# Kernel tuning notes

Hardware: AMD Instinct MI355X
Metric: run time of the kernel (lower is better)

The kernel has to match this reference:

```python
import jax, jax.numpy as jnp
import numpy as np

B, H, D, K, V, M = 64, 32, 4096, 128, 128, 4095

def setup_inputs() -> dict:
    key = jax.random.key(0)
    ks = jax.random.split(key, 7)
    return {
        "x": jax.random.normal(ks[0], (B, D), dtype=jnp.float32),
        "prev_K": jax.random.normal(ks[1], (B, M, K), dtype=jnp.float32),
        "prev_V": jax.random.normal(ks[2], (B, M, V), dtype=jnp.float32),
        "Wq": jax.random.normal(ks[3], (H, D, K), dtype=jnp.float32),
        "Wk": jax.random.normal(ks[4], (D, K), dtype=jnp.float32),
        "Wv": jax.random.normal(ks[5], (D, V), dtype=jnp.float32),
        "Wo": jax.random.normal(ks[6], (H, V, D), dtype=jnp.float32),
    }

def reference(x, prev_K, prev_V, Wq, Wk, Wv, Wo):
    # Projections
    q = jnp.einsum('bd,hdk->bhk', x, Wq)            # [b,h,k]
    k_new = jnp.einsum('bd,dk->bk', x, Wk)          # [b,k]
    v_new = jnp.einsum('bd,dv->bv', x, Wv)          # [b,v]
    Kc = jnp.concatenate([prev_K, k_new[:, None, :]], axis=1)  # [b,m+1,k]
    Vc = jnp.concatenate([prev_V, v_new[:, None, :]], axis=1)  # [b,m+1,v]
    # Shared-KV attention (MQA)
    logits = jnp.einsum('bhk,bmk->bhm', q, Kc)
    weights = jax.nn.softmax(logits, axis=-1)
    o = jnp.einsum('bhm,bmv->bhv', weights, Vc)
    y = jnp.einsum('bhv,hvd->bd', o, Wo)
    return (y, Kc, Vc)
```

## Files before the change

kernel.cpp:

```cpp
#include <hip/hip_runtime.h>
#include <stdint.h>

#define B_  64
#define H_  32
#define D_  4096
#define KD  128
#define VD  128
#define M_  4095
#define M1_ 4096
#define NCHUNK 32
#define LOG2E 1.44269504088896f

#define WS_P      0ull
#define WS_Q      4456448ull
#define WS_STATS  4718592ull
#define WS_O      4849664ull
#define WS_OPART  5111808ull

#define WAITVL(n) asm volatile("s_waitcnt vmcnt(" #n ") lgkmcnt(0)" ::: "memory")
#define WAITL()  asm volatile("s_waitcnt lgkmcnt(0)" ::: "memory")
#define BAR()    __builtin_amdgcn_s_barrier()

typedef __attribute__((address_space(3))) char lds_char;
typedef const __attribute__((address_space(1))) char glb_char;

__global__ __launch_bounds__(256) void k_proj_partial(
    const float* __restrict__ x, const float* __restrict__ Wq,
    const float* __restrict__ Wk, const float* __restrict__ Wv,
    float* __restrict__ P) {
  __shared__ float xs[64][260];
  const int dc = blockIdx.x;
  const int hx = blockIdx.y;
  const int t  = threadIdx.x;
  const float* xsrc = x + dc * 256;
  #pragma unroll
  for (int j = 0; j < 16; ++j) {
    int f = t + 256 * j;
    int row = f >> 6, c4 = f & 63;
    *(float4*)&xs[row][c4 * 4] =
        *(const float4*)(xsrc + (size_t)row * D_ + c4 * 4);
  }
  __syncthreads();
  const int bq = t >> 4;
  const int kg = t & 15;
  const int b0 = bq * 4;
  const float* W = (hx < H_) ? (Wq + (size_t)hx * D_ * KD)
                             : ((hx == H_) ? Wk : Wv);
  const float* wp = W + (size_t)(dc * 256) * KD + kg * 8;
  float acc[4][8];
  #pragma unroll
  for (int i = 0; i < 4; ++i)
    #pragma unroll
    for (int j = 0; j < 8; ++j) acc[i][j] = 0.f;
  #pragma unroll 8
  for (int d = 0; d < 256; ++d) {
    float4 w0 = *(const float4*)(wp + (size_t)d * KD);
    float4 w1 = *(const float4*)(wp + (size_t)d * KD + 4);
    float xv[4];
    #pragma unroll
    for (int i = 0; i < 4; ++i) xv[i] = xs[b0 + i][d];
    #pragma unroll
    for (int i = 0; i < 4; ++i) {
      acc[i][0] += xv[i] * w0.x; acc[i][1] += xv[i] * w0.y;
      acc[i][2] += xv[i] * w0.z; acc[i][3] += xv[i] * w0.w;
      acc[i][4] += xv[i] * w1.x; acc[i][5] += xv[i] * w1.y;
      acc[i][6] += xv[i] * w1.z; acc[i][7] += xv[i] * w1.w;
    }
  }
  #pragma unroll
  for (int i = 0; i < 4; ++i) {
    size_t base = ((size_t)(dc * 64 + b0 + i) * 34 + hx) * KD + kg * 8;
    *(float4*)&P[base]     = make_float4(acc[i][0], acc[i][1], acc[i][2], acc[i][3]);
    *(float4*)&P[base + 4] = make_float4(acc[i][4], acc[i][5], acc[i][6], acc[i][7]);
  }
}

__global__ __launch_bounds__(256) void k_proj_reduce(
    const float* __restrict__ P, float* __restrict__ q,
    float* __restrict__ Kc, float* __restrict__ Vc) {
  int i = blockIdx.x * 256 + threadIdx.x;
  int k = i & 127;
  int hx = (i >> 7) % 34;
  int b = i / (128 * 34);
  float s = 0.f;
  #pragma unroll
  for (int dc = 0; dc < 16; ++dc)
    s += P[(size_t)dc * (64 * 34 * 128) + (size_t)(b * 34 + hx) * 128 + k];
  if (hx < H_)       q[((size_t)b * H_ + hx) * KD + k] = s;
  else if (hx == H_) Kc[((size_t)b * M1_ + M_) * KD + k] = s;
  else               Vc[((size_t)b * M1_ + M_) * VD + k] = s;
}

__device__ __forceinline__ void stage_issue(
    const float* src, const float* app_row, float* lbuf, int m_lo, int t) {
  const int wb = t & ~63;
  #pragma unroll
  for (int j = 0; j < 4; ++j) {
    int f = j * 256 + t;
    int r = f >> 5, p = f & 31;
    int m = m_lo + r;
    int g4 = p ^ (r & 7);
    const float* gp = (m < M_) ? (src + (size_t)m * 128 + g4 * 4)
                               : (app_row + g4 * 4);
    __builtin_amdgcn_global_load_lds(
        (glb_char*)gp, (lds_char*)(lbuf + (size_t)(j * 256 + wb) * 4),
        16, 0, 0);
  }
}

__device__ __forceinline__ void copy_out(
    const float* lbuf, float* dst, int m_lo, int t) {
  #pragma unroll
  for (int jj = 0; jj < 4; ++jj) {
    int f = jj * 256 + t;
    int r = f >> 5, p = f & 31;
    int g4 = p ^ (r & 7);
    float4 v = *(const float4*)&lbuf[(size_t)f * 4];
    *(float4*)(dst + (size_t)(m_lo + r) * 128 + g4 * 4) = v;
  }
}

__global__ __launch_bounds__(256, 3) void k_flash(
    const float* __restrict__ prevK, const float* __restrict__ prevV,
    const float* __restrict__ q, float* __restrict__ Kc, float* __restrict__ Vc,
    float* __restrict__ o_part, float* __restrict__ stats) {
  __shared__ float buf[2][32 * 128];
  __shared__ float upool[4608];
  const int chunk = blockIdx.x;
  const int b = blockIdx.y;
  const int t = threadIdx.x;
  const int m0 = chunk * 128;

  const float* kbase = prevK + (size_t)b * M_ * KD;
  const float* vbase = prevV + (size_t)b * M_ * VD;
  const float* kapp  = Kc + ((size_t)b * M1_ + M_) * KD;
  const float* vapp  = Vc + ((size_t)b * M1_ + M_) * VD;
  float* kc = Kc + (size_t)b * M1_ * KD;
  float* vc = Vc + (size_t)b * M1_ * VD;

  const float* qsrc = q + (size_t)b * H_ * KD;
  float4 qv4[4];
  #pragma unroll
  for (int j = 0; j < 4; ++j) {
    int f = j * 256 + t;
    qv4[j] = *(const float4*)(qsrc + (size_t)(f >> 5) * KD + (f & 31) * 4);
  }
  stage_issue(kbase, kapp, buf[0], m0, t);
  #pragma unroll
  for (int j = 0; j < 4; ++j) {
    int f = j * 256 + t;
    *(float4*)&upool[(f >> 5) * 132 + (f & 31) * 4] = qv4[j];
  }

  const int mg = t & 15, hg = t >> 4, h0 = hg * 2;
  const int v4 = t & 31, hoct = t >> 5, h0v = hoct * 4;

  float accL0[8], accL1[8];

#define LOGITS_TILE(S, BUFI)                                                  \
  {                                                                           \
    const float* lb = buf[BUFI];                                              \
    float c00 = 0.f, c01 = 0.f, c10 = 0.f, c11 = 0.f;                         \
    const int sw = (mg & 7);                                                  \
    _Pragma("unroll 4")                                                       \
    for (int k4 = 0; k4 < 32; ++k4) {                                         \
      int p = (k4 ^ sw) * 4;                                                  \
      float4 qa = *(const float4*)&upool[h0 * 132 + k4 * 4];                  \
      float4 qb = *(const float4*)&upool[(h0 + 1) * 132 + k4 * 4];            \
      float4 k0v = *(const float4*)&lb[mg * 128 + p];                         \
      float4 k1v = *(const float4*)&lb[(mg + 16) * 128 + p];                  \
      c00 += qa.x*k0v.x + qa.y*k0v.y + qa.z*k0v.z + qa.w*k0v.w;               \
      c01 += qa.x*k1v.x + qa.y*k1v.y + qa.z*k1v.z + qa.w*k1v.w;               \
      c10 += qb.x*k0v.x + qb.y*k0v.y + qb.z*k0v.z + qb.w*k0v.w;               \
      c11 += qb.x*k1v.x + qb.y*k1v.y + qb.z*k1v.z + qb.w*k1v.w;               \
    }                                                                         \
    accL0[(S) * 2]     = c00;                                                 \
    accL0[(S) * 2 + 1] = c01;                                                 \
    accL1[(S) * 2]     = c10;                                                 \
    accL1[(S) * 2 + 1] = c11;                                                 \
  }

#define PV_TILE(S, BUFI)                                                      \
  {                                                                           \
    const float* lb = buf[BUFI];                                              \
    _Pragma("unroll 4")                                                       \
    for (int mm = 0; mm < 32; ++mm) {                                         \
      int p = (v4 ^ (mm & 7)) * 4;                                            \
      float4 gv = *(const float4*)&lb[mm * 128 + p];                          \
      float4 w4 = *(const float4*)&upool[((S) * 32 + mm) * 36 + h0v];         \
      a0.x += w4.x*gv.x; a0.y += w4.x*gv.y; a0.z += w4.x*gv.z; a0.w += w4.x*gv.w; \
      a1.x += w4.y*gv.x; a1.y += w4.y*gv.y; a1.z += w4.y*gv.z; a1.w += w4.y*gv.w; \
      a2.x += w4.z*gv.x; a2.y += w4.z*gv.y; a2.z += w4.z*gv.z; a2.w += w4.z*gv.w; \
      a3.x += w4.w*gv.x; a3.y += w4.w*gv.y; a3.z += w4.w*gv.z; a3.w += w4.w*gv.w; \
    }                                                                         \
  }

  stage_issue(kbase, kapp, buf[1], m0 + 32, t);
  WAITVL(4); BAR();
  LOGITS_TILE(0, 0);
  copy_out(buf[0], kc, m0, t);
  WAITL(); BAR();

  stage_issue(kbase, kapp, buf[0], m0 + 64, t);
  WAITVL(8); BAR();
  LOGITS_TILE(1, 1);
  copy_out(buf[1], kc, m0 + 32, t);
  WAITL(); BAR();

  stage_issue(kbase, kapp, buf[1], m0 + 96, t);
  WAITVL(8); BAR();
  LOGITS_TILE(2, 0);
  copy_out(buf[0], kc, m0 + 64, t);
  WAITL(); BAR();

  stage_issue(vbase, vapp, buf[0], m0, t);
  WAITVL(8); BAR();
  LOGITS_TILE(3, 1);
  copy_out(buf[1], kc, m0 + 96, t);
  WAITL(); BAR();

  {
    float mx0 = -3.402823466e38f, mx1 = -3.402823466e38f;
    #pragma unroll
    for (int j = 0; j < 8; ++j) {
      mx0 = fmaxf(mx0, accL0[j]);
      mx1 = fmaxf(mx1, accL1[j]);
    }
    #pragma unroll
    for (int off = 1; off <= 8; off <<= 1) {
      mx0 = fmaxf(mx0, __shfl_xor(mx0, off));
      mx1 = fmaxf(mx1, __shfl_xor(mx1, off));
    }
    float s0 = 0.f, s1 = 0.f;
    #pragma unroll
    for (int j = 0; j < 8; ++j) {
      float e0 = exp2f((accL0[j] - mx0) * LOG2E); accL0[j] = e0; s0 += e0;
      float e1 = exp2f((accL1[j] - mx1) * LOG2E); accL1[j] = e1; s1 += e1;
    }
    #pragma unroll
    for (int off = 1; off <= 8; off <<= 1) {
      s0 += __shfl_xor(s0, off);
      s1 += __shfl_xor(s1, off);
    }
    #pragma unroll
    for (int s = 0; s < 4; ++s)
      #pragma unroll
      for (int i = 0; i < 2; ++i) {
        int m = s * 32 + mg + 16 * i;
        upool[m * 36 + h0]     = accL0[s * 2 + i];
        upool[m * 36 + h0 + 1] = accL1[s * 2 + i];
      }
    if (mg == 0) {
      size_t sb0 = (((size_t)b * H_ + h0) * NCHUNK + chunk) * 2;
      *(float2*)&stats[sb0] = make_float2(mx0, s0);
      size_t sb1 = (((size_t)b * H_ + h0 + 1) * NCHUNK + chunk) * 2;
      *(float2*)&stats[sb1] = make_float2(mx1, s1);
    }
  }
  WAITL(); BAR();

  float4 a0 = {0,0,0,0}, a1 = {0,0,0,0}, a2 = {0,0,0,0}, a3 = {0,0,0,0};

  stage_issue(vbase, vapp, buf[1], m0 + 32, t);
  WAITVL(10); BAR();
  PV_TILE(0, 0);
  copy_out(buf[0], vc, m0, t);
  WAITL(); BAR();

  stage_issue(vbase, vapp, buf[0], m0 + 64, t);
  WAITVL(8); BAR();
  PV_TILE(1, 1);
  copy_out(buf[1], vc, m0 + 32, t);
  WAITL(); BAR();

  stage_issue(vbase, vapp, buf[1], m0 + 96, t);
  WAITVL(8); BAR();
  PV_TILE(2, 0);
  copy_out(buf[0], vc, m0 + 64, t);
  WAITL(); BAR();

  WAITVL(4); BAR();
  PV_TILE(3, 1);
  copy_out(buf[1], vc, m0 + 96, t);

  size_t base = ((size_t)(chunk * B_ + b) * H_ + h0v) * VD + v4 * 4;
  *(float4*)&o_part[base]          = a0;
  *(float4*)&o_part[base + VD]     = a1;
  *(float4*)&o_part[base + 2 * VD] = a2;
  *(float4*)&o_part[base + 3 * VD] = a3;
#undef LOGITS_TILE
#undef PV_TILE
}

__global__ __launch_bounds__(128) void k_combine(
    const float* __restrict__ o_part, const float* __restrict__ stats,
    float* __restrict__ o) {
  const int bh = blockIdx.x;
  const int t = threadIdx.x;
  __shared__ float st[64];
  if (t < 64) st[t] = stats[(size_t)bh * 64 + t];
  __syncthreads();
  float M = -3.402823466e38f;
  #pragma unroll
  for (int c = 0; c < NCHUNK; ++c) M = fmaxf(M, st[2 * c]);
  float wc[NCHUNK];
  float denom = 0.f;
  #pragma unroll
  for (int c = 0; c < NCHUNK; ++c) {
    float e = exp2f((st[2 * c] - M) * LOG2E);
    wc[c] = e;
    denom += st[2 * c + 1] * e;
  }
  const float inv = 1.0f / denom;
  const int b = bh >> 5, h = bh & 31;
  float acc = 0.f;
  #pragma unroll 4
  for (int c = 0; c < NCHUNK; ++c)
    acc += wc[c] * o_part[((size_t)(c * B_ + b) * H_ + h) * VD + t];
  o[(size_t)bh * VD + t] = acc * inv;
}

__global__ __launch_bounds__(256) void k_out_partial(
    const float* __restrict__ o, const float* __restrict__ Wo,
    float* __restrict__ Py) {
  __shared__ float os[64][260];
  const int dc = blockIdx.x;
  const int hvc = blockIdx.y;
  const int t = threadIdx.x;
  #pragma unroll
  for (int j = 0; j < 16; ++j) {
    int f = t + 256 * j;
    int row = f >> 6, c4 = f & 63;
    *(float4*)&os[row][c4 * 4] =
        *(const float4*)(o + (size_t)row * 4096 + hvc * 256 + c4 * 4);
  }
  __syncthreads();
  const int bq = t >> 4, dg = t & 15;
  const int b0 = bq * 4;
  const float* wp = Wo + (size_t)(hvc * 256) * D_ + dc * 128 + dg * 8;
  float acc[4][8];
  #pragma unroll
  for (int i = 0; i < 4; ++i)
    #pragma unroll
    for (int j = 0; j < 8; ++j) acc[i][j] = 0.f;
  #pragma unroll 8
  for (int hv = 0; hv < 256; ++hv) {
    float4 w0 = *(const float4*)(wp + (size_t)hv * D_);
    float4 w1 = *(const float4*)(wp + (size_t)hv * D_ + 4);
    float ov[4];
    #pragma unroll
    for (int i = 0; i < 4; ++i) ov[i] = os[b0 + i][hv];
    #pragma unroll
    for (int i = 0; i < 4; ++i) {
      acc[i][0] += ov[i] * w0.x; acc[i][1] += ov[i] * w0.y;
      acc[i][2] += ov[i] * w0.z; acc[i][3] += ov[i] * w0.w;
      acc[i][4] += ov[i] * w1.x; acc[i][5] += ov[i] * w1.y;
      acc[i][6] += ov[i] * w1.z; acc[i][7] += ov[i] * w1.w;
    }
  }
  #pragma unroll
  for (int i = 0; i < 4; ++i) {
    size_t base = ((size_t)hvc * 64 + b0 + i) * 4096 + dc * 128 + dg * 8;
    *(float4*)&Py[base]     = make_float4(acc[i][0], acc[i][1], acc[i][2], acc[i][3]);
    *(float4*)&Py[base + 4] = make_float4(acc[i][4], acc[i][5], acc[i][6], acc[i][7]);
  }
}

__global__ __launch_bounds__(256) void k_yreduce(
    const float* __restrict__ Py, float* __restrict__ y) {
  int i = blockIdx.x * 256 + threadIdx.x;
  float s = 0.f;
  #pragma unroll
  for (int c = 0; c < 16; ++c) s += Py[(size_t)c * 262144 + i];
  y[i] = s;
}

extern "C" void kernel_launch(void* const* d_in, const int* in_sizes, int n_in,
                              void* d_out, int out_size, void* d_ws, size_t ws_size,
                              hipStream_t stream) {
  const float* x     = (const float*)d_in[0];
  const float* prevK = (const float*)d_in[1];
  const float* prevV = (const float*)d_in[2];
  const float* Wq    = (const float*)d_in[3];
  const float* Wk    = (const float*)d_in[4];
  const float* Wv    = (const float*)d_in[5];
  const float* Wo    = (const float*)d_in[6];

  float* y  = (float*)d_out;
  float* Kc = y + (size_t)B_ * D_;
  float* Vc = Kc + (size_t)B_ * M1_ * KD;

  float* ws     = (float*)d_ws;
  float* P      = ws + WS_P;
  float* q      = ws + WS_Q;
  float* stats  = ws + WS_STATS;
  float* o      = ws + WS_O;
  float* o_part = ws + WS_OPART;

  k_proj_partial<<<dim3(16, 34), 256, 0, stream>>>(x, Wq, Wk, Wv, P);
  k_proj_reduce<<<1088, 256, 0, stream>>>(P, q, Kc, Vc);
  k_flash<<<dim3(32, 64), 256, 0, stream>>>(prevK, prevV, q, Kc, Vc, o_part, stats);
  k_combine<<<2048, 128, 0, stream>>>(o_part, stats, o);
  k_out_partial<<<dim3(32, 16), 256, 0, stream>>>(o, Wo, P);
  k_yreduce<<<1024, 256, 0, stream>>>(P, y);
}
```

Baseline: 263.8 us.

## Deepen K/V staging pipeline to four 16-row LDS buffers

Result: slower. 275.3 us (+4.4%).

```diff
diff --git a/kernel.cpp b/kernel.cpp
--- a/kernel.cpp
+++ b/kernel.cpp
@@ -95,7 +95,7 @@
     const float* src, const float* app_row, float* lbuf, int m_lo, int t) {
   const int wb = t & ~63;
   #pragma unroll
-  for (int j = 0; j < 4; ++j) {
+  for (int j = 0; j < 2; ++j) {
     int f = j * 256 + t;
     int r = f >> 5, p = f & 31;
     int m = m_lo + r;
@@ -111,7 +111,7 @@
 __device__ __forceinline__ void copy_out(
     const float* lbuf, float* dst, int m_lo, int t) {
   #pragma unroll
-  for (int jj = 0; jj < 4; ++jj) {
+  for (int jj = 0; jj < 2; ++jj) {
     int f = jj * 256 + t;
     int r = f >> 5, p = f & 31;
     int g4 = p ^ (r & 7);
@@ -124,7 +124,7 @@
     const float* __restrict__ prevK, const float* __restrict__ prevV,
     const float* __restrict__ q, float* __restrict__ Kc, float* __restrict__ Vc,
     float* __restrict__ o_part, float* __restrict__ stats) {
-  __shared__ float buf[2][32 * 128];
+  __shared__ float buf[4][16 * 128];
   __shared__ float upool[4608];
   const int chunk = blockIdx.x;
   const int b = blockIdx.y;
@@ -138,6 +138,12 @@
   float* kc = Kc + (size_t)b * M1_ * KD;
   float* vc = Vc + (size_t)b * M1_ * VD;
 
+#define STAGE16(g) stage_issue(((g) < 8 ? kbase : vbase),                     \
+                               ((g) < 8 ? kapp : vapp),                       \
+                               buf[(g) & 3], m0 + ((g) & 7) * 16, t)
+#define COPY16(g)  copy_out(buf[(g) & 3], ((g) < 8 ? kc : vc),                \
+                            m0 + ((g) & 7) * 16, t)
+
   const float* qsrc = q + (size_t)b * H_ * KD;
   float4 qv4[4];
   #pragma unroll
@@ -145,7 +151,7 @@
     int f = j * 256 + t;
     qv4[j] = *(const float4*)(qsrc + (size_t)(f >> 5) * KD + (f & 31) * 4);
   }
-  stage_issue(kbase, kapp, buf[0], m0, t);
+  STAGE16(0); STAGE16(1); STAGE16(2);
   #pragma unroll
   for (int j = 0; j < 4; ++j) {
     int f = j * 256 + t;
@@ -157,37 +163,31 @@
 
   float accL0[8], accL1[8];
 
-#define LOGITS_TILE(S, BUFI)                                                  \
+#define LOGITS16(G)                                                           \
   {                                                                           \
-    const float* lb = buf[BUFI];                                              \
-    float c00 = 0.f, c01 = 0.f, c10 = 0.f, c11 = 0.f;                         \
+    const float* lb = buf[(G) & 3];                                           \
+    float c0 = 0.f, c1 = 0.f;                                                 \
     const int sw = (mg & 7);                                                  \
-    _Pragma("unroll 4")                                                       \
+    _Pragma("unroll 8")                                                       \
     for (int k4 = 0; k4 < 32; ++k4) {                                         \
       int p = (k4 ^ sw) * 4;                                                  \
       float4 qa = *(const float4*)&upool[h0 * 132 + k4 * 4];                  \
       float4 qb = *(const float4*)&upool[(h0 + 1) * 132 + k4 * 4];            \
-      float4 k0v = *(const float4*)&lb[mg * 128 + p];                         \
-      float4 k1v = *(const float4*)&lb[(mg + 16) * 128 + p];                  \
-      c00 += qa.x*k0v.x + qa.y*k0v.y + qa.z*k0v.z + qa.w*k0v.w;               \
-      c01 += qa.x*k1v.x + qa.y*k1v.y + qa.z*k1v.z + qa.w*k1v.w;               \
-      c10 += qb.x*k0v.x + qb.y*k0v.y + qb.z*k0v.z + qb.w*k0v.w;               \
-      c11 += qb.x*k1v.x + qb.y*k1v.y + qb.z*k1v.z + qb.w*k1v.w;               \
+      float4 kv = *(const float4*)&lb[mg * 128 + p];                          \
+      c0 += qa.x*kv.x + qa.y*kv.y + qa.z*kv.z + qa.w*kv.w;                    \
+      c1 += qb.x*kv.x + qb.y*kv.y + qb.z*kv.z + qb.w*kv.w;                    \
     }                                                                         \
-    accL0[(S) * 2]     = c00;                                                 \
-    accL0[(S) * 2 + 1] = c01;                                                 \
-    accL1[(S) * 2]     = c10;                                                 \
-    accL1[(S) * 2 + 1] = c11;                                                 \
-  }
-
-#define PV_TILE(S, BUFI)                                                      \
+    accL0[G] = c0; accL1[G] = c1;                                             \
+  }
+
+#define PV16(G)                                                               \
   {                                                                           \
-    const float* lb = buf[BUFI];                                              \
-    _Pragma("unroll 4")                                                       \
-    for (int mm = 0; mm < 32; ++mm) {                                         \
+    const float* lb = buf[(G) & 3];                                           \
+    _Pragma("unroll 8")                                                       \
+    for (int mm = 0; mm < 16; ++mm) {                                         \
       int p = (v4 ^ (mm & 7)) * 4;                                            \
       float4 gv = *(const float4*)&lb[mm * 128 + p];                          \
-      float4 w4 = *(const float4*)&upool[((S) * 32 + mm) * 36 + h0v];         \
+      float4 w4 = *(const float4*)&upool[(((G) & 7) * 16 + mm) * 36 + h0v];   \
       a0.x += w4.x*gv.x; a0.y += w4.x*gv.y; a0.z += w4.x*gv.z; a0.w += w4.x*gv.w; \
       a1.x += w4.y*gv.x; a1.y += w4.y*gv.y; a1.z += w4.y*gv.z; a1.w += w4.y*gv.w; \
       a2.x += w4.z*gv.x; a2.y += w4.z*gv.y; a2.z += w4.z*gv.z; a2.w += w4.z*gv.w; \
@@ -195,28 +195,14 @@
     }                                                                         \
   }
 
-  stage_issue(kbase, kapp, buf[1], m0 + 32, t);
-  WAITVL(4); BAR();
-  LOGITS_TILE(0, 0);
-  copy_out(buf[0], kc, m0, t);
-  WAITL(); BAR();
-
-  stage_issue(kbase, kapp, buf[0], m0 + 64, t);
-  WAITVL(8); BAR();
-  LOGITS_TILE(1, 1);
-  copy_out(buf[1], kc, m0 + 32, t);
-  WAITL(); BAR();
-
-  stage_issue(kbase, kapp, buf[1], m0 + 96, t);
-  WAITVL(8); BAR();
-  LOGITS_TILE(2, 0);
-  copy_out(buf[0], kc, m0 + 64, t);
-  WAITL(); BAR();
-
-  stage_issue(vbase, vapp, buf[0], m0, t);
-  WAITVL(8); BAR();
-  LOGITS_TILE(3, 1);
-  copy_out(buf[1], kc, m0 + 96, t);
+  WAITVL(4);  BAR(); LOGITS16(0); COPY16(0); STAGE16(3);
+  WAITVL(6);  BAR(); LOGITS16(1); COPY16(1); STAGE16(4);
+  WAITVL(8);  BAR(); LOGITS16(2); COPY16(2); STAGE16(5);
+  WAITVL(8);  BAR(); LOGITS16(3); COPY16(3); STAGE16(6);
+  WAITVL(8);  BAR(); LOGITS16(4); COPY16(4); STAGE16(7);
+  WAITVL(8);  BAR(); LOGITS16(5); COPY16(5); STAGE16(8);
+  WAITVL(8);  BAR(); LOGITS16(6); COPY16(6); STAGE16(9);
+  WAITVL(8);  BAR(); LOGITS16(7); COPY16(7); STAGE16(10);
   WAITL(); BAR();
 
   {
@@ -243,13 +229,11 @@
       s1 += __shfl_xor(s1, off);
     }
     #pragma unroll
-    for (int s = 0; s < 4; ++s)
-      #pragma unroll
-      for (int i = 0; i < 2; ++i) {
-        int m = s * 32 + mg + 16 * i;
-        upool[m * 36 + h0]     = accL0[s * 2 + i];
-        upool[m * 36 + h0 + 1] = accL1[s * 2 + i];
-      }
+    for (int g = 0; g < 8; ++g) {
+      int m = g * 16 + mg;
+      upool[m * 36 + h0]     = accL0[g];
+      upool[m * 36 + h0 + 1] = accL1[g];
+    }
     if (mg == 0) {
       size_t sb0 = (((size_t)b * H_ + h0) * NCHUNK + chunk) * 2;
       *(float2*)&stats[sb0] = make_float2(mx0, s0);
@@ -261,35 +245,24 @@
 
   float4 a0 = {0,0,0,0}, a1 = {0,0,0,0}, a2 = {0,0,0,0}, a3 = {0,0,0,0};
 
-  stage_issue(vbase, vapp, buf[1], m0 + 32, t);
-  WAITVL(10); BAR();
-  PV_TILE(0, 0);
-  copy_out(buf[0], vc, m0, t);
-  WAITL(); BAR();
-
-  stage_issue(vbase, vapp, buf[0], m0 + 64, t);
-  WAITVL(8); BAR();
-  PV_TILE(1, 1);
-  copy_out(buf[1], vc, m0 + 32, t);
-  WAITL(); BAR();
-
-  stage_issue(vbase, vapp, buf[1], m0 + 96, t);
-  WAITVL(8); BAR();
-  PV_TILE(2, 0);
-  copy_out(buf[0], vc, m0 + 64, t);
-  WAITL(); BAR();
-
-  WAITVL(4); BAR();
-  PV_TILE(3, 1);
-  copy_out(buf[1], vc, m0 + 96, t);
+  WAITVL(10); BAR(); PV16(8);  COPY16(8);  STAGE16(11);
+  WAITVL(10); BAR(); PV16(9);  COPY16(9);  STAGE16(12);
+  WAITVL(10); BAR(); PV16(10); COPY16(10); STAGE16(13);
+  WAITVL(8);  BAR(); PV16(11); COPY16(11); STAGE16(14);
+  WAITVL(8);  BAR(); PV16(12); COPY16(12); STAGE16(15);
+  WAITVL(8);  BAR(); PV16(13); COPY16(13);
+  WAITVL(6);  BAR(); PV16(14); COPY16(14);
+  WAITVL(4);  BAR(); PV16(15); COPY16(15);
 
   size_t base = ((size_t)(chunk * B_ + b) * H_ + h0v) * VD + v4 * 4;
   *(float4*)&o_part[base]          = a0;
   *(float4*)&o_part[base + VD]     = a1;
   *(float4*)&o_part[base + 2 * VD] = a2;
   *(float4*)&o_part[base + 3 * VD] = a3;
-#undef LOGITS_TILE
-#undef PV_TILE
+#undef LOGITS16
+#undef PV16
+#undef STAGE16
+#undef COPY16
 }
 
 __global__ __launch_bounds__(128) void k_combine(
```

## Give each wave a private K slice to drop block barriers in logits phase

Applied to the files above, without the earlier changes.

New measurement: 270.9 us. +2.7%, slower.

```diff
diff --git a/kernel.cpp b/kernel.cpp
--- a/kernel.cpp
+++ b/kernel.cpp
@@ -90,6 +90,9 @@
   else if (hx == H_) Kc[((size_t)b * M1_ + M_) * KD + k] = s;
   else               Vc[((size_t)b * M1_ + M_) * VD + k] = s;
 }
+
+#define QSTRIDE 160
+#define QOFF(h) ((h) * QSTRIDE + ((((h) >> 1)) & 7) * 4)
 
 __device__ __forceinline__ void stage_issue(
     const float* src, const float* app_row, float* lbuf, int m_lo, int t) {
@@ -125,11 +128,13 @@
     const float* __restrict__ q, float* __restrict__ Kc, float* __restrict__ Vc,
     float* __restrict__ o_part, float* __restrict__ stats) {
   __shared__ float buf[2][32 * 128];
-  __shared__ float upool[4608];
+  __shared__ float upool[5120];
+  __shared__ float swl[4 * 64];
   const int chunk = blockIdx.x;
   const int b = blockIdx.y;
   const int t = threadIdx.x;
   const int m0 = chunk * 128;
+  const int w = t >> 6, l = t & 63;
 
   const float* kbase = prevK + (size_t)b * M_ * KD;
   const float* vbase = prevV + (size_t)b * M_ * VD;
@@ -138,6 +143,38 @@
   float* kc = Kc + (size_t)b * M1_ * KD;
   float* vc = Vc + (size_t)b * M1_ * VD;
 
+  float* kslice = &buf[0][0] + w * 2048;
+  const int mw = m0 + w * 32;
+
+#define KSTAGE(S)                                                             \
+  {                                                                           \
+    float* dst_ = kslice + ((S) & 1) * 1024;                                  \
+    _Pragma("unroll")                                                         \
+    for (int j = 0; j < 4; ++j) {                                             \
+      int f4 = j * 64 + l;                                                    \
+      int r = f4 >> 5, p = f4 & 31;                                           \
+      int m = mw + (S) * 8 + r;                                               \
+      int g4 = p ^ r;                                                         \
+      const float* gp = (m < M_) ? (kbase + (size_t)m * 128 + g4 * 4)         \
+                                 : (kapp + g4 * 4);                           \
+      __builtin_amdgcn_global_load_lds(                                       \
+          (glb_char*)gp, (lds_char*)(dst_ + j * 256), 16, 0, 0);              \
+    }                                                                         \
+  }
+
+#define KCOPY(S)                                                              \
+  {                                                                           \
+    const float* s_ = kslice + ((S) & 1) * 1024;                              \
+    _Pragma("unroll")                                                         \
+    for (int jj = 0; jj < 4; ++jj) {                                          \
+      int f4 = jj * 64 + l;                                                   \
+      int r = f4 >> 5, p = f4 & 31;                                           \
+      int g4 = p ^ r;                                                         \
+      float4 v = *(const float4*)&s_[f4 * 4];                                 \
+      *(float4*)(kc + (size_t)(mw + (S) * 8 + r) * 128 + g4 * 4) = v;         \
+    }                                                                         \
+  }
+
   const float* qsrc = q + (size_t)b * H_ * KD;
   float4 qv4[4];
   #pragma unroll
@@ -145,44 +182,42 @@
     int f = j * 256 + t;
     qv4[j] = *(const float4*)(qsrc + (size_t)(f >> 5) * KD + (f & 31) * 4);
   }
-  stage_issue(kbase, kapp, buf[0], m0, t);
+  KSTAGE(0); KSTAGE(1);
   #pragma unroll
   for (int j = 0; j < 4; ++j) {
     int f = j * 256 + t;
-    *(float4*)&upool[(f >> 5) * 132 + (f & 31) * 4] = qv4[j];
-  }
-
-  const int mg = t & 15, hg = t >> 4, h0 = hg * 2;
+    int row = f >> 5, c4 = f & 31;
+    *(float4*)&upool[QOFF(row) + c4 * 4] = qv4[j];
+  }
+
+  const int rp = l & 3, hg = l >> 2, h0 = hg * 2;
+  const int qA = QOFF(h0);
   const int v4 = t & 31, hoct = t >> 5, h0v = hoct * 4;
 
   float accL0[8], accL1[8];
 
-#define LOGITS_TILE(S, BUFI)                                                  \
+#define KLOG(S)                                                               \
   {                                                                           \
-    const float* lb = buf[BUFI];                                              \
+    const float* lb = kslice + ((S) & 1) * 1024;                              \
     float c00 = 0.f, c01 = 0.f, c10 = 0.f, c11 = 0.f;                         \
-    const int sw = (mg & 7);                                                  \
-    _Pragma("unroll 4")                                                       \
+    _Pragma("unroll 8")                                                       \
     for (int k4 = 0; k4 < 32; ++k4) {                                         \
-      int p = (k4 ^ sw) * 4;                                                  \
-      float4 qa = *(const float4*)&upool[h0 * 132 + k4 * 4];                  \
-      float4 qb = *(const float4*)&upool[(h0 + 1) * 132 + k4 * 4];            \
-      float4 k0v = *(const float4*)&lb[mg * 128 + p];                         \
-      float4 k1v = *(const float4*)&lb[(mg + 16) * 128 + p];                  \
+      float4 qa = *(const float4*)&upool[qA + k4 * 4];                        \
+      float4 qb = *(const float4*)&upool[qA + QSTRIDE + k4 * 4];              \
+      float4 k0v = *(const float4*)&lb[(rp * 32 + (k4 ^ rp)) * 4];            \
+      float4 k1v = *(const float4*)&lb[((rp + 4) * 32 + (k4 ^ (rp + 4))) * 4];\
       c00 += qa.x*k0v.x + qa.y*k0v.y + qa.z*k0v.z + qa.w*k0v.w;               \
       c01 += qa.x*k1v.x + qa.y*k1v.y + qa.z*k1v.z + qa.w*k1v.w;               \
       c10 += qb.x*k0v.x + qb.y*k0v.y + qb.z*k0v.z + qb.w*k0v.w;               \
       c11 += qb.x*k1v.x + qb.y*k1v.y + qb.z*k1v.z + qb.w*k1v.w;               \
     }                                                                         \
-    accL0[(S) * 2]     = c00;                                                 \
-    accL0[(S) * 2 + 1] = c01;                                                 \
-    accL1[(S) * 2]     = c10;                                                 \
-    accL1[(S) * 2 + 1] = c11;                                                 \
+    accL0[(S)*2] = c00; accL0[(S)*2+1] = c01;                                 \
+    accL1[(S)*2] = c10; accL1[(S)*2+1] = c11;                                 \
   }
 
 #define PV_TILE(S, BUFI)                                                      \
   {                                                                           \
-    const float* lb = buf[BUFI];                                              \
+    const float* lb = &buf[BUFI][0];                                          \
     _Pragma("unroll 4")                                                       \
     for (int mm = 0; mm < 32; ++mm) {                                         \
       int p = (v4 ^ (mm & 7)) * 4;                                            \
@@ -195,100 +230,89 @@
     }                                                                         \
   }
 
-  stage_issue(kbase, kapp, buf[1], m0 + 32, t);
+  WAITL(); BAR();
+
+  WAITVL(4);  KLOG(0); KCOPY(0); KSTAGE(2);
+  WAITVL(8);  KLOG(1); KCOPY(1); KSTAGE(3);
+  WAITVL(8);  KLOG(2); KCOPY(2);
+  WAITVL(4);  KLOG(3); KCOPY(3);
+
+  float mx0 = -3.402823466e38f, mx1 = -3.402823466e38f;
+  #pragma unroll
+  for (int j = 0; j < 8; ++j) {
+    mx0 = fmaxf(mx0, accL0[j]);
+    mx1 = fmaxf(mx1, accL1[j]);
+  }
+  mx0 = fmaxf(mx0, __shfl_xor(mx0, 1)); mx0 = fmaxf(mx0, __shfl_xor(mx0, 2));
+  mx1 = fmaxf(mx1, __shfl_xor(mx1, 1)); mx1 = fmaxf(mx1, __shfl_xor(mx1, 2));
+  float s0 = 0.f, s1 = 0.f;
+  #pragma unroll
+  for (int j = 0; j < 8; ++j) {
+    float e0 = exp2f((accL0[j] - mx0) * LOG2E); accL0[j] = e0; s0 += e0;
+    float e1 = exp2f((accL1[j] - mx1) * LOG2E); accL1[j] = e1; s1 += e1;
+  }
+  s0 += __shfl_xor(s0, 1); s0 += __shfl_xor(s0, 2);
+  s1 += __shfl_xor(s1, 1); s1 += __shfl_xor(s1, 2);
+  if (rp == 0)
+    *(float4*)&swl[w * 64 + h0 * 2] = make_float4(mx0, s0, mx1, s1);
+  WAITL(); BAR();
+
+  stage_issue(vbase, vapp, &buf[0][0], m0, t);
+  float cm0, cs0, cm1, cs1;
+  {
+    float4 r0 = *(const float4*)&swl[0 * 64 + h0 * 2];
+    float4 r1 = *(const float4*)&swl[1 * 64 + h0 * 2];
+    float4 r2 = *(const float4*)&swl[2 * 64 + h0 * 2];
+    float4 r3 = *(const float4*)&swl[3 * 64 + h0 * 2];
+    cm0 = fmaxf(fmaxf(r0.x, r1.x), fmaxf(r2.x, r3.x));
+    cm1 = fmaxf(fmaxf(r0.z, r1.z), fmaxf(r2.z, r3.z));
+    cs0 = r0.y * exp2f((r0.x - cm0) * LOG2E) + r1.y * exp2f((r1.x - cm0) * LOG2E)
+        + r2.y * exp2f((r2.x - cm0) * LOG2E) + r3.y * exp2f((r3.x - cm0) * LOG2E);
+    cs1 = r0.w * exp2f((r0.z - cm1) * LOG2E) + r1.w * exp2f((r1.z - cm1) * LOG2E)
+        + r2.w * exp2f((r2.z - cm1) * LOG2E) + r3.w * exp2f((r3.z - cm1) * LOG2E);
+    float f0 = exp2f((mx0 - cm0) * LOG2E);
+    float f1 = exp2f((mx1 - cm1) * LOG2E);
+    #pragma unroll
+    for (int S = 0; S < 4; ++S)
+      #pragma unroll
+      for (int half = 0; half < 2; ++half) {
+        int m = w * 32 + S * 8 + rp + 4 * half;
+        upool[m * 36 + h0]     = accL0[S * 2 + half] * f0;
+        upool[m * 36 + h0 + 1] = accL1[S * 2 + half] * f1;
+      }
+  }
+  stage_issue(vbase, vapp, &buf[1][0], m0 + 32, t);
   WAITVL(4); BAR();
-  LOGITS_TILE(0, 0);
-  copy_out(buf[0], kc, m0, t);
+
+  float4 a0 = {0,0,0,0}, a1 = {0,0,0,0}, a2 = {0,0,0,0}, a3 = {0,0,0,0};
+
+  PV_TILE(0, 0); copy_out(&buf[0][0], vc, m0, t);
   WAITL(); BAR();
-
-  stage_issue(kbase, kapp, buf[0], m0 + 64, t);
+  stage_issue(vbase, vapp, &buf[0][0], m0 + 64, t);
   WAITVL(8); BAR();
-  LOGITS_TILE(1, 1);
-  copy_out(buf[1], kc, m0 + 32, t);
+  PV_TILE(1, 1); copy_out(&buf[1][0], vc, m0 + 32, t);
   WAITL(); BAR();
-
-  stage_issue(kbase, kapp, buf[1], m0 + 96, t);
+  stage_issue(vbase, vapp, &buf[1][0], m0 + 96, t);
   WAITVL(8); BAR();
-  LOGITS_TILE(2, 0);
-  copy_out(buf[0], kc, m0 + 64, t);
-  WAITL(); BAR();
-
-  stage_issue(vbase, vapp, buf[0], m0, t);
-  WAITVL(8); BAR();
-  LOGITS_TILE(3, 1);
-  copy_out(buf[1], kc, m0 + 96, t);
-  WAITL(); BAR();
-
-  {
-    float mx0 = -3.402823466e38f, mx1 = -3.402823466e38f;
-    #pragma unroll
-    for (int j = 0; j < 8; ++j) {
-      mx0 = fmaxf(mx0, accL0[j]);
-      mx1 = fmaxf(mx1, accL1[j]);
-    }
-    #pragma unroll
-    for (int off = 1; off <= 8; off <<= 1) {
-      mx0 = fmaxf(mx0, __shfl_xor(mx0, off));
-      mx1 = fmaxf(mx1, __shfl_xor(mx1, off));
-    }
-    float s0 = 0.f, s1 = 0.f;
-    #pragma unroll
-    for (int j = 0; j < 8; ++j) {
-      float e0 = exp2f((accL0[j] - mx0) * LOG2E); accL0[j] = e0; s0 += e0;
-      float e1 = exp2f((accL1[j] - mx1) * LOG2E); accL1[j] = e1; s1 += e1;
-    }
-    #pragma unroll
-    for (int off = 1; off <= 8; off <<= 1) {
-      s0 += __shfl_xor(s0, off);
-      s1 += __shfl_xor(s1, off);
-    }
-    #pragma unroll
-    for (int s = 0; s < 4; ++s)
-      #pragma unroll
-      for (int i = 0; i < 2; ++i) {
-        int m = s * 32 + mg + 16 * i;
-        upool[m * 36 + h0]     = accL0[s * 2 + i];
-        upool[m * 36 + h0 + 1] = accL1[s * 2 + i];
-      }
-    if (mg == 0) {
-      size_t sb0 = (((size_t)b * H_ + h0) * NCHUNK + chunk) * 2;
-      *(float2*)&stats[sb0] = make_float2(mx0, s0);
-      size_t sb1 = (((size_t)b * H_ + h0 + 1) * NCHUNK + chunk) * 2;
-      *(float2*)&stats[sb1] = make_float2(mx1, s1);
-    }
-  }
-  WAITL(); BAR();
-
-  float4 a0 = {0,0,0,0}, a1 = {0,0,0,0}, a2 = {0,0,0,0}, a3 = {0,0,0,0};
-
-  stage_issue(vbase, vapp, buf[1], m0 + 32, t);
-  WAITVL(10); BAR();
-  PV_TILE(0, 0);
-  copy_out(buf[0], vc, m0, t);
-  WAITL(); BAR();
-
-  stage_issue(vbase, vapp, buf[0], m0 + 64, t);
-  WAITVL(8); BAR();
-  PV_TILE(1, 1);
-  copy_out(buf[1], vc, m0 + 32, t);
-  WAITL(); BAR();
-
-  stage_issue(vbase, vapp, buf[1], m0 + 96, t);
-  WAITVL(8); BAR();
-  PV_TILE(2, 0);
-  copy_out(buf[0], vc, m0 + 64, t);
-  WAITL(); BAR();
-
+  PV_TILE(2, 0); copy_out(&buf[0][0], vc, m0 + 64, t);
   WAITVL(4); BAR();
-  PV_TILE(3, 1);
-  copy_out(buf[1], vc, m0 + 96, t);
+  PV_TILE(3, 1); copy_out(&buf[1][0], vc, m0 + 96, t);
 
   size_t base = ((size_t)(chunk * B_ + b) * H_ + h0v) * VD + v4 * 4;
   *(float4*)&o_part[base]          = a0;
   *(float4*)&o_part[base + VD]     = a1;
   *(float4*)&o_part[base + 2 * VD] = a2;
   *(float4*)&o_part[base + 3 * VD] = a3;
-#undef LOGITS_TILE
+
+  if (w == 0 && rp == 0) {
+    size_t sb0 = (((size_t)b * H_ + h0) * NCHUNK + chunk) * 2;
+    *(float2*)&stats[sb0] = make_float2(cm0, cs0);
+    size_t sb1 = (((size_t)b * H_ + h0 + 1) * NCHUNK + chunk) * 2;
+    *(float2*)&stats[sb1] = make_float2(cm1, cs1);
+  }
+#undef KSTAGE
+#undef KCOPY
+#undef KLOG
 #undef PV_TILE
 }
 
```
